# Kernel tuning notes

Hardware: AMD Instinct MI355X
Metric: run time of the kernel (lower is better)

Reference implementation:

```python
import jax, jax.numpy as jnp
import numpy as np

N_NODES = 100000   # graph size
N_EDGES = 1200000  # ~avg degree 12
D_IN = 256
D_OUT = 64


def setup_inputs() -> dict:
    key = jax.random.key(0)
    k1, k2, k3, k4, k5 = jax.random.split(key, 5)
    X = jax.random.normal(k1, (N_NODES, D_IN), dtype=jnp.float32)
    # xavier_uniform-ish scale for W
    limit = np.sqrt(6.0 / (D_IN + D_OUT)).astype(np.float32)
    W = jax.random.uniform(k2, (D_IN, D_OUT), dtype=jnp.float32, minval=-limit, maxval=limit)
    A_rows = jax.random.randint(k3, (N_EDGES,), 0, N_NODES, dtype=jnp.int32)
    A_cols = jax.random.randint(k4, (N_EDGES,), 0, N_NODES, dtype=jnp.int32)
    A_vals = jax.random.uniform(k5, (N_EDGES,), dtype=jnp.float32)  # normalized adjacency weights
    return {"X": X, "W": W, "A_rows": A_rows, "A_cols": A_cols, "A_vals": A_vals}


def reference(X, W, A_rows, A_cols, A_vals) -> jnp.ndarray:
    # support = X @ W  (feature transform; torch.sparse.mm(X, W))
    support = X @ W  # [N, D_OUT]
    # A @ support in COO form: gather source-node features, scale by edge weight,
    # scatter-add into destination rows (torch.sparse.mm(A, support)).
    msgs = A_vals[:, None] * support[A_cols]          # [E, D_OUT]
    out = jax.ops.segment_sum(msgs, A_rows, num_segments=N_NODES)  # [N, D_OUT]
    return out
```

## Files before the change

kernel.cpp:

```cpp
#include <hip/hip_runtime.h>

#define N_NODES 100000
#define N_EDGES 1200000
#define D_IN 256
#define D_OUT 64

#define BUCKET_BITS 5
#define BUCKET_ROWS 32
#define N_BUCKETS   (N_NODES / BUCKET_ROWS)
#define NBLK_E      640
#define EPB         (N_EDGES / NBLK_E)
#define N_GROUPS    196
#define CPL         10
#define CAP         1536

#define C2D_IDX(b, k) ((((size_t)((b) >> 4) * NBLK_E + (k)) << 4) | ((b) & 15))

#define OFF_SUPPORT   0u
#define OFF_BSUM      12800000u
#define OFF_BBASE     12812544u
#define OFF_ETMP      12825088u
#define OFF_EDGEG     22425088u
#define OFF_C2D       OFF_EDGEG
#define WS_NEEDED     32025088u

using bf16x8 = __attribute__((ext_vector_type(8))) short;
using f32x4  = __attribute__((ext_vector_type(4))) float;

static __device__ __forceinline__ ushort f32_to_bf16_rne(float f) {
    unsigned bits = __float_as_uint(f);
    unsigned r = (bits + 0x7FFFu + ((bits >> 16) & 1u)) >> 16;
    return (ushort)r;
}
static __device__ __forceinline__ float bf16_to_f32(ushort u) {
    return __uint_as_float((unsigned)u << 16);
}
static __device__ __forceinline__ unsigned pack2bf(float a, float b) {
    return (unsigned)f32_to_bf16_rne(a) | ((unsigned)f32_to_bf16_rne(b) << 16);
}

__global__ __launch_bounds__(256, 4) void gemm_xw_mfma(const float* __restrict__ X,
                                                       const float* __restrict__ W,
                                                       ushort* __restrict__ support) {
    __shared__ ushort XsT[4][128][8];
    __shared__ ushort WtT[32][64][8];

    const int t = threadIdx.x;
    const int lane = t & 63;
    const int w = t >> 6;
    const int lr = lane & 15;
    const int lg = lane >> 4;

#pragma unroll
    for (int p = 0; p < 16; ++p) {
        int idx = t + p * 256;
        int k   = idx >> 4;
        int c4  = idx & 15;
        float4 v = *reinterpret_cast<const float4*>(W + (size_t)k * D_OUT + c4 * 4);
        WtT[k >> 3][c4 * 4 + 0][k & 7] = f32_to_bf16_rne(v.x);
        WtT[k >> 3][c4 * 4 + 1][k & 7] = f32_to_bf16_rne(v.y);
        WtT[k >> 3][c4 * 4 + 2][k & 7] = f32_to_bf16_rne(v.z);
        WtT[k >> 3][c4 * 4 + 3][k & 7] = f32_to_bf16_rne(v.w);
    }

    int xrow[4], xq[4];
#pragma unroll
    for (int p = 0; p < 4; ++p) {
        int idx = t + p * 256;
        xrow[p] = idx >> 3;
        xq[p]   = idx & 7;
    }

    for (int tile = 0; tile < 2; ++tile) {
        const int row0 = blockIdx.x * 256 + tile * 128;
        if (row0 >= N_NODES) break;

        bool xval[4];
#pragma unroll
        for (int p = 0; p < 4; ++p) xval[p] = (row0 + xrow[p]) < N_NODES;

        float4 xreg[4];
#pragma unroll
        for (int p = 0; p < 4; ++p) {
            xreg[p] = make_float4(0.f, 0.f, 0.f, 0.f);
            if (xval[p])
                xreg[p] = *reinterpret_cast<const float4*>(
                    X + (size_t)(row0 + xrow[p]) * D_IN + xq[p] * 4);
        }

        f32x4 acc[2][4];
#pragma unroll
        for (int mi = 0; mi < 2; ++mi)
#pragma unroll
            for (int ni = 0; ni < 4; ++ni) acc[mi][ni] = (f32x4){0.f, 0.f, 0.f, 0.f};

        for (int kt = 0; kt < 8; ++kt) {
#pragma unroll
            for (int p = 0; p < 4; ++p) {
                uint2 u;
                u.x = pack2bf(xreg[p].x, xreg[p].y);
                u.y = pack2bf(xreg[p].z, xreg[p].w);
                *reinterpret_cast<uint2*>(&XsT[xq[p] >> 1][xrow[p]][(xq[p] & 1) * 4]) = u;
            }
            __syncthreads();

            if (kt < 7) {
#pragma unroll
                for (int p = 0; p < 4; ++p) {
                    if (xval[p])
                        xreg[p] = *reinterpret_cast<const float4*>(
                            X + (size_t)(row0 + xrow[p]) * D_IN + (kt + 1) * 32 + xq[p] * 4);
                }
            }

            bf16x8 a0 = *reinterpret_cast<const bf16x8*>(&XsT[lg][w * 32 + lr][0]);
            bf16x8 a1 = *reinterpret_cast<const bf16x8*>(&XsT[lg][w * 32 + 16 + lr][0]);
#pragma unroll
            for (int ni = 0; ni < 4; ++ni) {
                bf16x8 b = *reinterpret_cast<const bf16x8*>(&WtT[kt * 4 + lg][ni * 16 + lr][0]);
                acc[0][ni] = __builtin_amdgcn_mfma_f32_16x16x32_bf16(a0, b, acc[0][ni], 0, 0, 0);
                acc[1][ni] = __builtin_amdgcn_mfma_f32_16x16x32_bf16(a1, b, acc[1][ni], 0, 0, 0);
            }
            __syncthreads();
        }

#pragma unroll
        for (int mi = 0; mi < 2; ++mi) {
#pragma unroll
            for (int reg = 0; reg < 4; ++reg) {
                int grow = row0 + w * 32 + mi * 16 + lg * 4 + reg;
                if (grow < N_NODES) {
#pragma unroll
                    for (int ni = 0; ni < 4; ++ni)
                        support[(size_t)grow * D_OUT + ni * 16 + lr] =
                            f32_to_bf16_rne(acc[mi][ni][reg]);
                }
            }
        }
    }
}

__global__ __launch_bounds__(256) void bucket_count(const int* __restrict__ rows,
                                                    int* __restrict__ c2d) {
    __shared__ int h[N_BUCKETS];
    for (int i = threadIdx.x; i < N_BUCKETS; i += 256) h[i] = 0;
    __syncthreads();
    const int base = blockIdx.x * EPB;
    for (int i = threadIdx.x; i < EPB; i += 256)
        atomicAdd(&h[rows[base + i] >> BUCKET_BITS], 1);
    __syncthreads();
    const int k = blockIdx.x;
    for (int b = threadIdx.x; b < N_GROUPS * 16; b += 256)
        c2d[C2D_IDX(b, k)] = (b < N_BUCKETS) ? h[b] : 0;
}

__global__ __launch_bounds__(256) void scan_groups(int* __restrict__ c2d,
                                                   int* __restrict__ bsum) {
    __shared__ int T[16][NBLK_E + 4];
    const int t = threadIdx.x;
    const int w = t >> 6;
    const int l = t & 63;
    const size_t base = (size_t)blockIdx.x * NBLK_E * 16;

    for (int i = t; i < NBLK_E * 16; i += 256) {
        int k = i >> 4, bl = i & 15;
        T[bl][k] = c2d[base + i];
    }
    __syncthreads();

#pragma unroll
    for (int q = 0; q < 4; ++q) {
        const int bl = w * 4 + q;
        int loc[CPL];
        int sum = 0;
#pragma unroll
        for (int j = 0; j < CPL; ++j) {
            int v = T[bl][l * CPL + j];
            loc[j] = sum;
            sum += v;
        }
        int s = sum;
#pragma unroll
        for (int off = 1; off < 64; off <<= 1) {
            int u = __shfl_up(s, off);
            if (l >= off) s += u;
        }
        if (l == 63) bsum[blockIdx.x * 16 + bl] = s;
        int ex = s - sum;
#pragma unroll
        for (int j = 0; j < CPL; ++j)
            T[bl][l * CPL + j] = ex + loc[j];
    }
    __syncthreads();

    for (int i = t; i < NBLK_E * 16; i += 256) {
        int k = i >> 4, bl = i & 15;
        c2d[base + i] = T[bl][k];
    }
}

__global__ __launch_bounds__(256) void bucket_scatter3(const int* __restrict__ rows,
                                                       const int* __restrict__ cols,
                                                       const float* __restrict__ vals,
                                                       const int* __restrict__ c2d,
                                                       const int* __restrict__ bsum,
                                                       int* __restrict__ bbase,
                                                       uint2* __restrict__ etmp) {
    __shared__ int s[256];
    __shared__ int off[N_BUCKETS];
    const int t = threadIdx.x;
    const int blk = blockIdx.x;

    int loc[13];
    int sum = 0;
#pragma unroll
    for (int j = 0; j < 13; ++j) {
        int idx = t * 13 + j;
        int v = (idx < N_BUCKETS) ? bsum[idx] : 0;
        loc[j] = sum;
        sum += v;
    }
    s[t] = sum;
    __syncthreads();
#pragma unroll
    for (int o = 1; o < 256; o <<= 1) {
        int x = (t >= o) ? s[t - o] : 0;
        __syncthreads();
        s[t] += x;
        __syncthreads();
    }
    int base0 = s[t] - sum;
#pragma unroll
    for (int j = 0; j < 13; ++j) {
        int idx = t * 13 + j;
        if (idx < N_BUCKETS) {
            int bb = base0 + loc[j];
            off[idx] = bb + c2d[C2D_IDX(idx, blk)];
            if (blk == 0) bbase[idx] = bb;
        }
    }
    __syncthreads();

    const int base = blk * EPB;
    for (int i = t; i < EPB; i += 256) {
        int e = base + i;
        int r = rows[e];
        int b = r >> BUCKET_BITS;
        int pos = atomicAdd(&off[b], 1);
        etmp[pos] = make_uint2((unsigned)cols[e] |
                               ((unsigned)(r & (BUCKET_ROWS - 1)) << 17),
                               __float_as_uint(vals[e]));
    }
}

__global__ __launch_bounds__(256) void sort_gather(const uint2* __restrict__ etmp,
                                                   const int* __restrict__ bbase,
                                                   const int* __restrict__ bsum,
                                                   const ushort* __restrict__ support,
                                                   uint2* __restrict__ edge_g,
                                                   float* __restrict__ out) {
    __shared__ uint2 eL[CAP];
    __shared__ int cnt[BUCKET_ROWS], pos[BUCKET_ROWS], fill[BUCKET_ROWS];
    const int t = threadIdx.x;
    const int lane = t & 63;
    const int w = t >> 6;
    const int b = blockIdx.x;
    const int r0 = b << BUCKET_BITS;
    const int s0 = bbase[b];
    const int n  = bsum[b];

    if (t < BUCKET_ROWS) cnt[t] = 0;
    __syncthreads();

    for (int i = t; i < n; i += 256)
        atomicAdd(&cnt[etmp[s0 + i].x >> 17], 1);
    __syncthreads();

    if (t < 64) {
        int v = (t < 32) ? cnt[t] : 0;
        int s = v;
#pragma unroll
        for (int off = 1; off < 32; off <<= 1) {
            int u = __shfl_up(s, off);
            if (lane >= off) s += u;
        }
        if (t < 32) { pos[t] = s - v; fill[t] = 0; }
    }
    __syncthreads();

    const bool inLDS = (n <= CAP);
    if (inLDS) {
        for (int i = t; i < n; i += 256) {
            uint2 u = etmp[s0 + i];
            int r = (int)(u.x >> 17);
            int p = pos[r] + atomicAdd(&fill[r], 1);
            eL[p] = make_uint2(u.x & 0x1FFFFu, u.y);
        }
    } else {
        for (int i = t; i < n; i += 256) {
            uint2 u = etmp[s0 + i];
            int r = (int)(u.x >> 17);
            int p = pos[r] + atomicAdd(&fill[r], 1);
            edge_g[s0 + p] = make_uint2(u.x & 0x1FFFFu, u.y);
        }
    }
    __syncthreads();

    const int h = lane >> 5;
    const int c = lane & 31;

#define GATHER_BODY(SRC)                                                          \
    for (int rr = w; rr < BUCKET_ROWS; rr += 4) {                                 \
        int e = pos[rr], end = pos[rr] + cnt[rr];                                 \
        float2 acc = {0.f, 0.f};                                                  \
        for (; e + 3 < end; e += 4) {                                             \
            uint2 p0 = SRC(e + h);                                                \
            uint2 p1 = SRC(e + 2 + h);                                            \
            unsigned s0v = *reinterpret_cast<const unsigned*>(                    \
                support + (size_t)p0.x * D_OUT + 2 * c);                          \
            unsigned s1v = *reinterpret_cast<const unsigned*>(                    \
                support + (size_t)p1.x * D_OUT + 2 * c);                          \
            float v0 = __uint_as_float(p0.y);                                     \
            float v1 = __uint_as_float(p1.y);                                     \
            acc.x = fmaf(v0, bf16_to_f32((ushort)(s0v & 0xFFFFu)), acc.x);        \
            acc.y = fmaf(v0, bf16_to_f32((ushort)(s0v >> 16)), acc.y);            \
            acc.x = fmaf(v1, bf16_to_f32((ushort)(s1v & 0xFFFFu)), acc.x);        \
            acc.y = fmaf(v1, bf16_to_f32((ushort)(s1v >> 16)), acc.y);            \
        }                                                                         \
        for (int ee = e + h; ee < end; ee += 2) {                                 \
            uint2 p = SRC(ee);                                                    \
            unsigned sv = *reinterpret_cast<const unsigned*>(                     \
                support + (size_t)p.x * D_OUT + 2 * c);                           \
            float v = __uint_as_float(p.y);                                       \
            acc.x = fmaf(v, bf16_to_f32((ushort)(sv & 0xFFFFu)), acc.x);          \
            acc.y = fmaf(v, bf16_to_f32((ushort)(sv >> 16)), acc.y);              \
        }                                                                         \
        acc.x += __shfl_xor(acc.x, 32);                                           \
        acc.y += __shfl_xor(acc.y, 32);                                           \
        if (h == 0)                                                               \
            *reinterpret_cast<float2*>(out + (size_t)(r0 + rr) * D_OUT + 2 * c) = acc; \
    }

    if (inLDS) {
#define SRCL(i) eL[i]
        GATHER_BODY(SRCL)
#undef SRCL
    } else {
        const uint2* eg = edge_g + s0;
#define SRCG(i) eg[i]
        GATHER_BODY(SRCG)
#undef SRCG
    }
#undef GATHER_BODY
}

__global__ void zero_out(float4* __restrict__ out, int n4) {
    int i = blockIdx.x * blockDim.x + threadIdx.x;
    int stride = gridDim.x * blockDim.x;
    for (; i < n4; i += stride) out[i] = float4{0.0f, 0.0f, 0.0f, 0.0f};
}

__global__ __launch_bounds__(256) void spmm_scatter(const int* __restrict__ rows,
                                                    const int* __restrict__ cols,
                                                    const float* __restrict__ vals,
                                                    const ushort* __restrict__ support,
                                                    float* __restrict__ out,
                                                    int n_edges) {
    const int lane = threadIdx.x & 63;
    const int wave_global = (int)((blockIdx.x * blockDim.x + threadIdx.x) >> 6);
    const int n_waves = (int)((gridDim.x * blockDim.x) >> 6);

    for (int base = wave_global * 64; base < n_edges; base += n_waves * 64) {
        int my_e = base + lane;
        int r = rows[my_e];
        int c = cols[my_e];
        float v = vals[my_e];

        int cnt = min(64, n_edges - base);
        for (int i = 0; i < cnt; ++i) {
            int row = __shfl(r, i);
            int col = __shfl(c, i);
            float val = __shfl(v, i);
            float s = bf16_to_f32(support[(size_t)col * D_OUT + lane]);
            atomicAdd(&out[(size_t)row * D_OUT + lane], val * s);
        }
    }
}

extern "C" void kernel_launch(void* const* d_in, const int* in_sizes, int n_in,
                              void* d_out, int out_size, void* d_ws, size_t ws_size,
                              hipStream_t stream) {
    const float* X      = (const float*)d_in[0];
    const float* W      = (const float*)d_in[1];
    const int*   A_rows = (const int*)d_in[2];
    const int*   A_cols = (const int*)d_in[3];
    const float* A_vals = (const float*)d_in[4];
    float* out = (float*)d_out;

    char* ws = (char*)d_ws;
    ushort* support = (ushort*)(ws + OFF_SUPPORT);

    const int gemm_blocks = (N_NODES + 255) / 256;

    if (ws_size >= (size_t)WS_NEEDED) {
        int*   bsum   = (int*)(ws + OFF_BSUM);
        int*   bbase  = (int*)(ws + OFF_BBASE);
        int*   c2d    = (int*)(ws + OFF_C2D);
        uint2* etmp   = (uint2*)(ws + OFF_ETMP);
        uint2* edge_g = (uint2*)(ws + OFF_EDGEG);

        bucket_count<<<NBLK_E, 256, 0, stream>>>(A_rows, c2d);
        scan_groups<<<N_GROUPS, 256, 0, stream>>>(c2d, bsum);
        bucket_scatter3<<<NBLK_E, 256, 0, stream>>>(A_rows, A_cols, A_vals,
                                                    c2d, bsum, bbase, etmp);
        gemm_xw_mfma<<<gemm_blocks, 256, 0, stream>>>(X, W, support);
        sort_gather<<<N_BUCKETS, 256, 0, stream>>>(etmp, bbase, bsum,
                                                   support, edge_g, out);
    } else {
        int n4 = (N_NODES * D_OUT) / 4;
        zero_out<<<2048, 256, 0, stream>>>((float4*)out, n4);
        gemm_xw_mfma<<<gemm_blocks, 256, 0, stream>>>(X, W, support);
        int chunks = N_EDGES / 64;
        spmm_scatter<<<(chunks + 3) / 4, 256, 0, stream>>>(A_rows, A_cols, A_vals,
                                                           support, out, N_EDGES);
    }
}
```

Before: 111.9 us.

## Load X fragments directly into MFMA registers, drop LDS staging for X

The GEMM kernel no longer stages X tiles through shared memory with two barriers per k-step. Each lane now loads its own 8 consecutive floats per row straight from global memory, packs them to bf16 and feeds them to MFMA. The W transpose is rewritten to use per-column scalar loads with 16-byte LDS stores, and each block now covers 128 rows instead of looping over two 128-row tiles, so twice as many blocks launch. The trade is less synchronisation and LDS traffic against 32-byte-per-lane global X loads that may coalesce less well, and W is converted once per 128 rows instead of once per 256.

```diff
diff --git a/kernel.cpp b/kernel.cpp
--- a/kernel.cpp
+++ b/kernel.cpp
@@ -39,10 +39,9 @@
     return (unsigned)f32_to_bf16_rne(a) | ((unsigned)f32_to_bf16_rne(b) << 16);
 }
 
-__global__ __launch_bounds__(256, 4) void gemm_xw_mfma(const float* __restrict__ X,
-                                                       const float* __restrict__ W,
-                                                       ushort* __restrict__ support) {
-    __shared__ ushort XsT[4][128][8];
+__global__ __launch_bounds__(256) void gemm_xw_mfma(const float* __restrict__ X,
+                                                    const float* __restrict__ W,
+                                                    ushort* __restrict__ support) {
     __shared__ ushort WtT[32][64][8];
 
     const int t = threadIdx.x;
@@ -50,91 +49,76 @@
     const int w = t >> 6;
     const int lr = lane & 15;
     const int lg = lane >> 4;
-
-#pragma unroll
-    for (int p = 0; p < 16; ++p) {
-        int idx = t + p * 256;
-        int k   = idx >> 4;
-        int c4  = idx & 15;
-        float4 v = *reinterpret_cast<const float4*>(W + (size_t)k * D_OUT + c4 * 4);
-        WtT[k >> 3][c4 * 4 + 0][k & 7] = f32_to_bf16_rne(v.x);
-        WtT[k >> 3][c4 * 4 + 1][k & 7] = f32_to_bf16_rne(v.y);
-        WtT[k >> 3][c4 * 4 + 2][k & 7] = f32_to_bf16_rne(v.z);
-        WtT[k >> 3][c4 * 4 + 3][k & 7] = f32_to_bf16_rne(v.w);
-    }
-
-    int xrow[4], xq[4];
-#pragma unroll
-    for (int p = 0; p < 4; ++p) {
-        int idx = t + p * 256;
-        xrow[p] = idx >> 3;
-        xq[p]   = idx & 7;
-    }
-
-    for (int tile = 0; tile < 2; ++tile) {
-        const int row0 = blockIdx.x * 256 + tile * 128;
-        if (row0 >= N_NODES) break;
-
-        bool xval[4];
-#pragma unroll
-        for (int p = 0; p < 4; ++p) xval[p] = (row0 + xrow[p]) < N_NODES;
-
-        float4 xreg[4];
-#pragma unroll
-        for (int p = 0; p < 4; ++p) {
-            xreg[p] = make_float4(0.f, 0.f, 0.f, 0.f);
-            if (xval[p])
-                xreg[p] = *reinterpret_cast<const float4*>(
-                    X + (size_t)(row0 + xrow[p]) * D_IN + xq[p] * 4);
-        }
-
-        f32x4 acc[2][4];
-#pragma unroll
-        for (int mi = 0; mi < 2; ++mi)
-#pragma unroll
-            for (int ni = 0; ni < 4; ++ni) acc[mi][ni] = (f32x4){0.f, 0.f, 0.f, 0.f};
-
-        for (int kt = 0; kt < 8; ++kt) {
-#pragma unroll
-            for (int p = 0; p < 4; ++p) {
-                uint2 u;
-                u.x = pack2bf(xreg[p].x, xreg[p].y);
-                u.y = pack2bf(xreg[p].z, xreg[p].w);
-                *reinterpret_cast<uint2*>(&XsT[xq[p] >> 1][xrow[p]][(xq[p] & 1) * 4]) = u;
-            }
-            __syncthreads();
-
-            if (kt < 7) {
-#pragma unroll
-                for (int p = 0; p < 4; ++p) {
-                    if (xval[p])
-                        xreg[p] = *reinterpret_cast<const float4*>(
-                            X + (size_t)(row0 + xrow[p]) * D_IN + (kt + 1) * 32 + xq[p] * 4);
-                }
-            }
-
-            bf16x8 a0 = *reinterpret_cast<const bf16x8*>(&XsT[lg][w * 32 + lr][0]);
-            bf16x8 a1 = *reinterpret_cast<const bf16x8*>(&XsT[lg][w * 32 + 16 + lr][0]);
-#pragma unroll
-            for (int ni = 0; ni < 4; ++ni) {
-                bf16x8 b = *reinterpret_cast<const bf16x8*>(&WtT[kt * 4 + lg][ni * 16 + lr][0]);
-                acc[0][ni] = __builtin_amdgcn_mfma_f32_16x16x32_bf16(a0, b, acc[0][ni], 0, 0, 0);
-                acc[1][ni] = __builtin_amdgcn_mfma_f32_16x16x32_bf16(a1, b, acc[1][ni], 0, 0, 0);
-            }
-            __syncthreads();
-        }
-
-#pragma unroll
-        for (int mi = 0; mi < 2; ++mi) {
-#pragma unroll
-            for (int reg = 0; reg < 4; ++reg) {
-                int grow = row0 + w * 32 + mi * 16 + lg * 4 + reg;
-                if (grow < N_NODES) {
-#pragma unroll
-                    for (int ni = 0; ni < 4; ++ni)
-                        support[(size_t)grow * D_OUT + ni * 16 + lr] =
-                            f32_to_bf16_rne(acc[mi][ni][reg]);
-                }
+    const int row0 = blockIdx.x * 128;
+
+    {
+        const int c   = t & 63;
+        const int kg0 = t >> 6;
+#pragma unroll
+        for (int i = 0; i < 8; ++i) {
+            int kg = kg0 + i * 4;
+            uint4 u;
+            u.x = pack2bf(W[(size_t)(kg * 8 + 0) * D_OUT + c],
+                          W[(size_t)(kg * 8 + 1) * D_OUT + c]);
+            u.y = pack2bf(W[(size_t)(kg * 8 + 2) * D_OUT + c],
+                          W[(size_t)(kg * 8 + 3) * D_OUT + c]);
+            u.z = pack2bf(W[(size_t)(kg * 8 + 4) * D_OUT + c],
+                          W[(size_t)(kg * 8 + 5) * D_OUT + c]);
+            u.w = pack2bf(W[(size_t)(kg * 8 + 6) * D_OUT + c],
+                          W[(size_t)(kg * 8 + 7) * D_OUT + c]);
+            *reinterpret_cast<uint4*>(&WtT[kg][c][0]) = u;
+        }
+    }
+    __syncthreads();
+
+    const int ra0 = row0 + w * 32 + lr;
+    const int ra1 = ra0 + 16;
+    const bool v0 = ra0 < N_NODES;
+    const bool v1 = ra1 < N_NODES;
+    const float* pa0 = X + (size_t)ra0 * D_IN + lg * 8;
+    const float* pa1 = X + (size_t)ra1 * D_IN + lg * 8;
+
+    f32x4 acc[2][4];
+#pragma unroll
+    for (int mi = 0; mi < 2; ++mi)
+#pragma unroll
+        for (int ni = 0; ni < 4; ++ni) acc[mi][ni] = (f32x4){0.f, 0.f, 0.f, 0.f};
+
+    const float4 z4 = make_float4(0.f, 0.f, 0.f, 0.f);
+
+#pragma unroll
+    for (int kt = 0; kt < 8; ++kt) {
+        float4 x00 = v0 ? *reinterpret_cast<const float4*>(pa0 + kt * 32)     : z4;
+        float4 x01 = v0 ? *reinterpret_cast<const float4*>(pa0 + kt * 32 + 4) : z4;
+        float4 x10 = v1 ? *reinterpret_cast<const float4*>(pa1 + kt * 32)     : z4;
+        float4 x11 = v1 ? *reinterpret_cast<const float4*>(pa1 + kt * 32 + 4) : z4;
+
+        uint4 ua, ub;
+        ua.x = pack2bf(x00.x, x00.y); ua.y = pack2bf(x00.z, x00.w);
+        ua.z = pack2bf(x01.x, x01.y); ua.w = pack2bf(x01.z, x01.w);
+        ub.x = pack2bf(x10.x, x10.y); ub.y = pack2bf(x10.z, x10.w);
+        ub.z = pack2bf(x11.x, x11.y); ub.w = pack2bf(x11.z, x11.w);
+        bf16x8 a0 = *reinterpret_cast<bf16x8*>(&ua);
+        bf16x8 a1 = *reinterpret_cast<bf16x8*>(&ub);
+
+#pragma unroll
+        for (int ni = 0; ni < 4; ++ni) {
+            bf16x8 b = *reinterpret_cast<const bf16x8*>(&WtT[kt * 4 + lg][ni * 16 + lr][0]);
+            acc[0][ni] = __builtin_amdgcn_mfma_f32_16x16x32_bf16(a0, b, acc[0][ni], 0, 0, 0);
+            acc[1][ni] = __builtin_amdgcn_mfma_f32_16x16x32_bf16(a1, b, acc[1][ni], 0, 0, 0);
+        }
+    }
+
+#pragma unroll
+    for (int mi = 0; mi < 2; ++mi) {
+#pragma unroll
+        for (int reg = 0; reg < 4; ++reg) {
+            int grow = row0 + w * 32 + mi * 16 + lg * 4 + reg;
+            if (grow < N_NODES) {
+#pragma unroll
+                for (int ni = 0; ni < 4; ++ni)
+                    support[(size_t)grow * D_OUT + ni * 16 + lr] =
+                        f32_to_bf16_rne(acc[mi][ni][reg]);
             }
         }
     }
@@ -400,7 +384,7 @@
     char* ws = (char*)d_ws;
     ushort* support = (ushort*)(ws + OFF_SUPPORT);
 
-    const int gemm_blocks = (N_NODES + 255) / 256;
+    const int gemm_blocks = (N_NODES + 127) / 128;
 
     if (ws_size >= (size_t)WS_NEEDED) {
         int*   bsum   = (int*)(ws + OFF_BSUM);
```

New measurement: 138.2 us. 23.5% more time.

## Precompute bf16 W once and double-buffer X tiles in GEMM

Applied to the files above, without the earlier changes.

W is converted to bf16 in a pre-transposed fragment layout once, by extra blocks appended to the bucket_count launch, and stored in the workspace. The GEMM then reads B fragments straight from global memory (cached) instead of having every block rebuild a 32KB LDS copy of W. The GEMM now handles one 128-row tile per block and double-buffers the X LDS stage so the next tile is staged after the MFMAs, leaving one barrier per k-step. This removes redundant W conversion and LDS pressure, which should raise occupancy, at the cost of global-memory B loads inside the inner loop.

```diff
diff --git a/kernel.cpp b/kernel.cpp
--- a/kernel.cpp
+++ b/kernel.cpp
@@ -19,10 +19,11 @@
 #define OFF_SUPPORT   0u
 #define OFF_BSUM      12800000u
 #define OFF_BBASE     12812544u
-#define OFF_ETMP      12825088u
-#define OFF_EDGEG     22425088u
+#define OFF_WBF       12825088u
+#define OFF_ETMP      12857856u
+#define OFF_EDGEG     22457856u
 #define OFF_C2D       OFF_EDGEG
-#define WS_NEEDED     32025088u
+#define WS_NEEDED     32057856u
 
 using bf16x8 = __attribute__((ext_vector_type(8))) short;
 using f32x4  = __attribute__((ext_vector_type(4))) float;
@@ -39,119 +40,131 @@
     return (unsigned)f32_to_bf16_rne(a) | ((unsigned)f32_to_bf16_rne(b) << 16);
 }
 
-__global__ __launch_bounds__(256, 4) void gemm_xw_mfma(const float* __restrict__ X,
-                                                       const float* __restrict__ W,
-                                                       ushort* __restrict__ support) {
-    __shared__ ushort XsT[4][128][8];
-    __shared__ ushort WtT[32][64][8];
+static __device__ __forceinline__ void wprep_body(int kb, int t,
+                                                  const float* __restrict__ W,
+                                                  ushort* __restrict__ Wbf) {
+    const int c  = t & 63;
+    const int kg = kb * 4 + (t >> 6);
+    uint4 u;
+    u.x = pack2bf(W[(size_t)(kg * 8 + 0) * D_OUT + c], W[(size_t)(kg * 8 + 1) * D_OUT + c]);
+    u.y = pack2bf(W[(size_t)(kg * 8 + 2) * D_OUT + c], W[(size_t)(kg * 8 + 3) * D_OUT + c]);
+    u.z = pack2bf(W[(size_t)(kg * 8 + 4) * D_OUT + c], W[(size_t)(kg * 8 + 5) * D_OUT + c]);
+    u.w = pack2bf(W[(size_t)(kg * 8 + 6) * D_OUT + c], W[(size_t)(kg * 8 + 7) * D_OUT + c]);
+    *reinterpret_cast<uint4*>(Wbf + ((size_t)kg * 64 + c) * 8) = u;
+}
+
+__global__ __launch_bounds__(256) void gemm_xw_mfma(const float* __restrict__ X,
+                                                    const ushort* __restrict__ Wbf,
+                                                    ushort* __restrict__ support) {
+    __shared__ ushort Xs[2][4][128][8];
 
     const int t = threadIdx.x;
     const int lane = t & 63;
     const int w = t >> 6;
     const int lr = lane & 15;
     const int lg = lane >> 4;
-
-#pragma unroll
-    for (int p = 0; p < 16; ++p) {
-        int idx = t + p * 256;
-        int k   = idx >> 4;
-        int c4  = idx & 15;
-        float4 v = *reinterpret_cast<const float4*>(W + (size_t)k * D_OUT + c4 * 4);
-        WtT[k >> 3][c4 * 4 + 0][k & 7] = f32_to_bf16_rne(v.x);
-        WtT[k >> 3][c4 * 4 + 1][k & 7] = f32_to_bf16_rne(v.y);
-        WtT[k >> 3][c4 * 4 + 2][k & 7] = f32_to_bf16_rne(v.z);
-        WtT[k >> 3][c4 * 4 + 3][k & 7] = f32_to_bf16_rne(v.w);
-    }
-
-    int xrow[4], xq[4];
+    const int row0 = blockIdx.x * 128;
+
+    int  xrow[4], xq[4];
+    bool xval[4];
 #pragma unroll
     for (int p = 0; p < 4; ++p) {
         int idx = t + p * 256;
         xrow[p] = idx >> 3;
         xq[p]   = idx & 7;
-    }
-
-    for (int tile = 0; tile < 2; ++tile) {
-        const int row0 = blockIdx.x * 256 + tile * 128;
-        if (row0 >= N_NODES) break;
-
-        bool xval[4];
-#pragma unroll
-        for (int p = 0; p < 4; ++p) xval[p] = (row0 + xrow[p]) < N_NODES;
-
-        float4 xreg[4];
-#pragma unroll
-        for (int p = 0; p < 4; ++p) {
-            xreg[p] = make_float4(0.f, 0.f, 0.f, 0.f);
-            if (xval[p])
-                xreg[p] = *reinterpret_cast<const float4*>(
-                    X + (size_t)(row0 + xrow[p]) * D_IN + xq[p] * 4);
-        }
-
-        f32x4 acc[2][4];
-#pragma unroll
-        for (int mi = 0; mi < 2; ++mi)
-#pragma unroll
-            for (int ni = 0; ni < 4; ++ni) acc[mi][ni] = (f32x4){0.f, 0.f, 0.f, 0.f};
-
-        for (int kt = 0; kt < 8; ++kt) {
+        xval[p] = (row0 + xrow[p]) < N_NODES;
+    }
+
+    float4 xreg[4];
+#pragma unroll
+    for (int p = 0; p < 4; ++p) {
+        xreg[p] = make_float4(0.f, 0.f, 0.f, 0.f);
+        if (xval[p])
+            xreg[p] = *reinterpret_cast<const float4*>(
+                X + (size_t)(row0 + xrow[p]) * D_IN + xq[p] * 4);
+    }
+
+#define STAGE_X(buf)                                                              \
+    {                                                                             \
+        _Pragma("unroll")                                                         \
+        for (int p = 0; p < 4; ++p) {                                             \
+            uint2 u;                                                              \
+            u.x = pack2bf(xreg[p].x, xreg[p].y);                                  \
+            u.y = pack2bf(xreg[p].z, xreg[p].w);                                  \
+            *reinterpret_cast<uint2*>(&Xs[buf][xq[p] >> 1][xrow[p]][(xq[p] & 1) * 4]) = u; \
+        }                                                                         \
+    }
+
+    STAGE_X(0)
+    __syncthreads();
+
+    f32x4 acc[2][4];
+#pragma unroll
+    for (int mi = 0; mi < 2; ++mi)
+#pragma unroll
+        for (int ni = 0; ni < 4; ++ni) acc[mi][ni] = (f32x4){0.f, 0.f, 0.f, 0.f};
+
+#pragma unroll
+    for (int kt = 0; kt < 8; ++kt) {
+        const int cur = kt & 1;
+
+        if (kt < 7) {
 #pragma unroll
             for (int p = 0; p < 4; ++p) {
-                uint2 u;
-                u.x = pack2bf(xreg[p].x, xreg[p].y);
-                u.y = pack2bf(xreg[p].z, xreg[p].w);
-                *reinterpret_cast<uint2*>(&XsT[xq[p] >> 1][xrow[p]][(xq[p] & 1) * 4]) = u;
+                if (xval[p])
+                    xreg[p] = *reinterpret_cast<const float4*>(
+                        X + (size_t)(row0 + xrow[p]) * D_IN + (kt + 1) * 32 + xq[p] * 4);
             }
-            __syncthreads();
-
-            if (kt < 7) {
-#pragma unroll
-                for (int p = 0; p < 4; ++p) {
-                    if (xval[p])
-                        xreg[p] = *reinterpret_cast<const float4*>(
-                            X + (size_t)(row0 + xrow[p]) * D_IN + (kt + 1) * 32 + xq[p] * 4);
-                }
+        }
+
+        bf16x8 a0 = *reinterpret_cast<const bf16x8*>(&Xs[cur][lg][w * 32 + lr][0]);
+        bf16x8 a1 = *reinterpret_cast<const bf16x8*>(&Xs[cur][lg][w * 32 + 16 + lr][0]);
+        const ushort* wb = Wbf + ((size_t)(kt * 4 + lg) * 64) * 8;
+#pragma unroll
+        for (int ni = 0; ni < 4; ++ni) {
+            bf16x8 b = *reinterpret_cast<const bf16x8*>(wb + (size_t)(ni * 16 + lr) * 8);
+            acc[0][ni] = __builtin_amdgcn_mfma_f32_16x16x32_bf16(a0, b, acc[0][ni], 0, 0, 0);
+            acc[1][ni] = __builtin_amdgcn_mfma_f32_16x16x32_bf16(a1, b, acc[1][ni], 0, 0, 0);
+        }
+
+        if (kt < 7) STAGE_X(cur ^ 1)
+        __syncthreads();
+    }
+#undef STAGE_X
+
+#pragma unroll
+    for (int mi = 0; mi < 2; ++mi) {
+#pragma unroll
+        for (int reg = 0; reg < 4; ++reg) {
+            int grow = row0 + w * 32 + mi * 16 + lg * 4 + reg;
+            if (grow < N_NODES) {
+#pragma unroll
+                for (int ni = 0; ni < 4; ++ni)
+                    support[(size_t)grow * D_OUT + ni * 16 + lr] =
+                        f32_to_bf16_rne(acc[mi][ni][reg]);
             }
-
-            bf16x8 a0 = *reinterpret_cast<const bf16x8*>(&XsT[lg][w * 32 + lr][0]);
-            bf16x8 a1 = *reinterpret_cast<const bf16x8*>(&XsT[lg][w * 32 + 16 + lr][0]);
-#pragma unroll
-            for (int ni = 0; ni < 4; ++ni) {
-                bf16x8 b = *reinterpret_cast<const bf16x8*>(&WtT[kt * 4 + lg][ni * 16 + lr][0]);
-                acc[0][ni] = __builtin_amdgcn_mfma_f32_16x16x32_bf16(a0, b, acc[0][ni], 0, 0, 0);
-                acc[1][ni] = __builtin_amdgcn_mfma_f32_16x16x32_bf16(a1, b, acc[1][ni], 0, 0, 0);
-            }
-            __syncthreads();
-        }
-
-#pragma unroll
-        for (int mi = 0; mi < 2; ++mi) {
-#pragma unroll
-            for (int reg = 0; reg < 4; ++reg) {
-                int grow = row0 + w * 32 + mi * 16 + lg * 4 + reg;
-                if (grow < N_NODES) {
-#pragma unroll
-                    for (int ni = 0; ni < 4; ++ni)
-                        support[(size_t)grow * D_OUT + ni * 16 + lr] =
-                            f32_to_bf16_rne(acc[mi][ni][reg]);
-                }
-            }
         }
     }
 }
 
 __global__ __launch_bounds__(256) void bucket_count(const int* __restrict__ rows,
-                                                    int* __restrict__ c2d) {
+                                                    int* __restrict__ c2d,
+                                                    const float* __restrict__ W,
+                                                    ushort* __restrict__ Wbf) {
     __shared__ int h[N_BUCKETS];
+    const int bid = blockIdx.x;
+    if (bid >= NBLK_E) {
+        wprep_body(bid - NBLK_E, threadIdx.x, W, Wbf);
+        return;
+    }
     for (int i = threadIdx.x; i < N_BUCKETS; i += 256) h[i] = 0;
     __syncthreads();
-    const int base = blockIdx.x * EPB;
+    const int base = bid * EPB;
     for (int i = threadIdx.x; i < EPB; i += 256)
         atomicAdd(&h[rows[base + i] >> BUCKET_BITS], 1);
     __syncthreads();
-    const int k = blockIdx.x;
     for (int b = threadIdx.x; b < N_GROUPS * 16; b += 256)
-        c2d[C2D_IDX(b, k)] = (b < N_BUCKETS) ? h[b] : 0;
+        c2d[C2D_IDX(b, bid)] = (b < N_BUCKETS) ? h[b] : 0;
 }
 
 __global__ __launch_bounds__(256) void scan_groups(int* __restrict__ c2d,
@@ -354,6 +367,11 @@
 #undef GATHER_BODY
 }
 
+__global__ __launch_bounds__(256) void wprep_standalone(const float* __restrict__ W,
+                                                        ushort* __restrict__ Wbf) {
+    wprep_body(blockIdx.x, threadIdx.x, W, Wbf);
+}
+
 __global__ void zero_out(float4* __restrict__ out, int n4) {
     int i = blockIdx.x * blockDim.x + threadIdx.x;
     int stride = gridDim.x * blockDim.x;
@@ -399,8 +417,9 @@
 
     char* ws = (char*)d_ws;
     ushort* support = (ushort*)(ws + OFF_SUPPORT);
-
-    const int gemm_blocks = (N_NODES + 255) / 256;
+    ushort* Wbf     = (ushort*)(ws + OFF_WBF);
+
+    const int gemm_blocks = (N_NODES + 127) / 128;
 
     if (ws_size >= (size_t)WS_NEEDED) {
         int*   bsum   = (int*)(ws + OFF_BSUM);
@@ -409,17 +428,18 @@
         uint2* etmp   = (uint2*)(ws + OFF_ETMP);
         uint2* edge_g = (uint2*)(ws + OFF_EDGEG);
 
-        bucket_count<<<NBLK_E, 256, 0, stream>>>(A_rows, c2d);
+        bucket_count<<<NBLK_E + 8, 256, 0, stream>>>(A_rows, c2d, W, Wbf);
         scan_groups<<<N_GROUPS, 256, 0, stream>>>(c2d, bsum);
         bucket_scatter3<<<NBLK_E, 256, 0, stream>>>(A_rows, A_cols, A_vals,
                                                     c2d, bsum, bbase, etmp);
-        gemm_xw_mfma<<<gemm_blocks, 256, 0, stream>>>(X, W, support);
+        gemm_xw_mfma<<<gemm_blocks, 256, 0, stream>>>(X, Wbf, support);
         sort_gather<<<N_BUCKETS, 256, 0, stream>>>(etmp, bbase, bsum,
                                                    support, edge_g, out);
     } else {
+        wprep_standalone<<<8, 256, 0, stream>>>(W, Wbf);
         int n4 = (N_NODES * D_OUT) / 4;
         zero_out<<<2048, 256, 0, stream>>>((float4*)out, n4);
-        gemm_xw_mfma<<<gemm_blocks, 256, 0, stream>>>(X, W, support);
+        gemm_xw_mfma<<<gemm_blocks, 256, 0, stream>>>(X, Wbf, support);
         int chunks = N_EDGES / 64;
         spmm_scatter<<<(chunks + 3) / 4, 256, 0, stream>>>(A_rows, A_cols, A_vals,
                                                            support, out, N_EDGES);
```

After: 111.4 us. Within noise of the previous version (-0.5%).
